# Kernel tuning notes

Measured on AMD Instinct MI355X. Metric: run time of the kernel, lower is better.

Reference implementation:

```python
import jax, jax.numpy as jnp
import numpy as np

EMBED_DIM = 512
N_QUERY = 4096
N_PROTO = 1024


def setup_inputs() -> dict:
    key = jax.random.key(0)
    k_q, k_p, k_wmu = jax.random.split(key, 3)
    d = EMBED_DIM
    bound = (6.0 / (d + d)) ** 0.5
    return {
        "query_features": jax.random.normal(k_q, (N_QUERY, d), dtype=jnp.float32),
        "prototypes": jax.random.normal(k_p, (N_PROTO, d), dtype=jnp.float32),
        "weight_mu": jax.random.uniform(k_wmu, (d, d), dtype=jnp.float32, minval=-bound, maxval=bound),
        "weight_rho": jnp.full((d, d), -3.0, dtype=jnp.float32),
        "bias_mu": jnp.zeros((d,), dtype=jnp.float32),
        "bias_rho": jnp.full((d,), 0.01, dtype=jnp.float32),
        "n_samples": 10,
    }


def reference(query_features, prototypes, weight_mu, weight_rho, bias_mu, bias_rho, n_samples):
    d = weight_mu.shape[0]
    # softplus reparameterization (same each iteration in the original loop)
    weight_sigma = jnp.log1p(jnp.exp(weight_rho))  # [d, d]
    bias_sigma = jnp.log1p(jnp.exp(bias_rho))      # [d]
    # batched MC weight/bias samples: [S, d, d] and [S, d]
    key = jax.random.key(42)
    kw, kb = jax.random.split(key)
    eps_w = jax.random.normal(kw, (n_samples, d, d), dtype=weight_mu.dtype)
    eps_b = jax.random.normal(kb, (n_samples, d), dtype=bias_mu.dtype)
    w = weight_mu[None] + weight_sigma[None] * eps_w   # [S, d, d]
    b = bias_mu[None] + bias_sigma[None] * eps_b       # [S, d]
    # F.linear(x, W_sample.T, b) == x @ W_sample + b
    tq = jnp.einsum('qd,sde->sqe', query_features, w) + b[:, None, :]  # [S, Q, d]
    # cdist via ||a||^2 + ||b||^2 - 2 a.b
    sq_q = jnp.sum(tq * tq, axis=-1)                    # [S, Q]
    sq_p = jnp.sum(prototypes * prototypes, axis=-1)    # [P]
    cross = jnp.einsum('sqe,pe->sqp', tq, prototypes)   # [S, Q, P]
    sqd = sq_q[:, :, None] + sq_p[None, None, :] - 2.0 * cross
    dists = jnp.sqrt(jnp.maximum(sqd, 1e-12))           # [S, Q, P]
    mean_distance = jnp.mean(dists, axis=0)
    uncertainty = jnp.std(dists, axis=0, ddof=1)        # torch.std is unbiased
    return mean_distance, uncertainty
```

## Files before the change

kernel.cpp:

```cpp
#include <hip/hip_runtime.h>
#include <stdint.h>

#define NS 10
#define DIM 512
#define NQ 4096
#define NP 1024

typedef unsigned short ushort_t;
typedef __bf16 bf16el_t;
typedef bf16el_t bf16x8 __attribute__((ext_vector_type(8)));
typedef float floatx4 __attribute__((ext_vector_type(4)));

__host__ __device__ __forceinline__ uint32_t rotl32(uint32_t x, int r) {
  return (x << r) | (x >> (32 - r));
}

__host__ __device__ __forceinline__ void threefry2x32(uint32_t k0, uint32_t k1,
                                                      uint32_t x0, uint32_t x1,
                                                      uint32_t* o0, uint32_t* o1) {
  uint32_t ks2 = k0 ^ k1 ^ 0x1BD11BDAu;
  x0 += k0; x1 += k1;
#define TF_R(r) { x0 += x1; x1 = rotl32(x1, r); x1 ^= x0; }
  TF_R(13) TF_R(15) TF_R(26) TF_R(6)   x0 += k1;  x1 += ks2 + 1u;
  TF_R(17) TF_R(29) TF_R(16) TF_R(24)  x0 += ks2; x1 += k0 + 2u;
  TF_R(13) TF_R(15) TF_R(26) TF_R(6)   x0 += k0;  x1 += k1 + 3u;
  TF_R(17) TF_R(29) TF_R(16) TF_R(24)  x0 += k1;  x1 += ks2 + 4u;
  TF_R(13) TF_R(15) TF_R(26) TF_R(6)   x0 += ks2; x1 += k0 + 5u;
#undef TF_R
  *o0 = x0; *o1 = x1;
}

__device__ __forceinline__ uint32_t jax_random_bits(uint32_t k0, uint32_t k1, uint32_t idx) {
  uint32_t o0, o1;
  threefry2x32(k0, k1, 0u, idx, &o0, &o1);
  return o0 ^ o1;
}

__device__ __forceinline__ float erfinvf_xla(float x) {
  float w = -log1pf(-x * x);
  float p;
  if (w < 5.0f) {
    w -= 2.5f;
    p = 2.81022636e-08f;
    p = fmaf(p, w, 3.43273939e-07f);
    p = fmaf(p, w, -3.5233877e-06f);
    p = fmaf(p, w, -4.39150654e-06f);
    p = fmaf(p, w, 0.00021858087f);
    p = fmaf(p, w, -0.00125372503f);
    p = fmaf(p, w, -0.00417768164f);
    p = fmaf(p, w, 0.246640727f);
    p = fmaf(p, w, 1.50140941f);
  } else {
    w = sqrtf(w) - 3.0f;
    p = -0.000200214257f;
    p = fmaf(p, w, 0.000100950558f);
    p = fmaf(p, w, 0.00134934322f);
    p = fmaf(p, w, -0.00367342844f);
    p = fmaf(p, w, 0.00573950773f);
    p = fmaf(p, w, -0.0076224613f);
    p = fmaf(p, w, 0.00943887047f);
    p = fmaf(p, w, 1.00167406f);
    p = fmaf(p, w, 2.83297682f);
  }
  return p * x;
}

__device__ __forceinline__ float jax_bits_to_normal(uint32_t bits) {
  float f = __uint_as_float((bits >> 9) | 0x3F800000u) - 1.0f;
  float u = f * 2.0f - 0.99999994f;
  u = fmaxf(u, -0.99999994f);
  return 1.41421356f * erfinvf_xla(u);
}

__device__ __forceinline__ float softplusf(float x) { return log1pf(expf(x)); }

__device__ __forceinline__ float bf2f(ushort_t u) {
  return __uint_as_float(((uint32_t)u) << 16);
}
__device__ __forceinline__ ushort_t f2bf(float f) {
  uint32_t u = __float_as_uint(f);
  u += 0x7FFFu + ((u >> 16) & 1u);
  return (ushort_t)(u >> 16);
}

__device__ __forceinline__ void gll16(const void* g, void* l) {
  __builtin_amdgcn_global_load_lds(
      (const __attribute__((address_space(1))) uint32_t*)g,
      (__attribute__((address_space(3))) uint32_t*)l, 16, 0, 0);
}

__global__ __launch_bounds__(256) void prep_kernel(const float* __restrict__ qf,
                                                   const float* __restrict__ pf,
                                                   const float* __restrict__ wmu,
                                                   const float* __restrict__ wrho,
                                                   const float* __restrict__ bmu,
                                                   const float* __restrict__ brho,
                                                   ushort_t* __restrict__ wt,
                                                   ushort_t* __restrict__ qb,
                                                   ushort_t* __restrict__ pb,
                                                   float* __restrict__ sqp,
                                                   float* __restrict__ bvec,
                                                   float* __restrict__ sqq,
                                                   uint32_t kw0, uint32_t kw1,
                                                   uint32_t kb0, uint32_t kb1) {
  const int blk = blockIdx.x;
  const int tid = threadIdx.x;
  if (blk < 10240) {
    uint32_t t = blk * 256u + tid;
    uint32_t s = t >> 18;
    uint32_t r = t & 0x3FFFFu;
    uint32_t e = r >> 9;
    uint32_t k = r & 511u;
    uint32_t eps_idx = (s << 18) | (k << 9) | e;
    uint32_t bits = jax_random_bits(kw0, kw1, eps_idx);
    float n = jax_bits_to_normal(bits);
    uint32_t mi = (k << 9) | e;
    float w = wmu[mi] + softplusf(wrho[mi]) * n;
    wt[t] = f2bf(w);
  } else if (blk < 12288) {
    int i = ((blk - 10240) * 256 + tid) * 4;
    float4 v = *(const float4*)&qf[i];
    uint2 r;
    r.x = (uint32_t)f2bf(v.x) | ((uint32_t)f2bf(v.y) << 16);
    r.y = (uint32_t)f2bf(v.z) | ((uint32_t)f2bf(v.w) << 16);
    *(uint2*)&qb[i] = r;
  } else if (blk < 12544) {
    int p = (blk - 12288) * 4 + (tid >> 6);
    int lane = tid & 63;
    const float* src = pf + p * DIM + lane * 8;
    float4 a = *(const float4*)src;
    float4 b = *(const float4*)(src + 4);
    float vals[8] = {a.x, a.y, a.z, a.w, b.x, b.y, b.z, b.w};
    ushort_t o[8];
    float ss = 0.f;
#pragma unroll
    for (int i = 0; i < 8; ++i) {
      o[i] = f2bf(vals[i]);
      float f = bf2f(o[i]);
      ss += f * f;
    }
    *(uint4*)&pb[p * DIM + lane * 8] = *(const uint4*)o;
#pragma unroll
    for (int off = 32; off; off >>= 1) ss += __shfl_xor(ss, off, 64);
    if (lane == 0) sqp[p] = ss;
  } else if (blk < 12564) {
    uint32_t t2 = (blk - 12544) * 256u + tid;
    uint32_t e = t2 & 511u;
    uint32_t bits = jax_random_bits(kb0, kb1, t2);
    float n = jax_bits_to_normal(bits);
    bvec[t2] = bmu[e] + softplusf(brho[e]) * n;
  } else {
    int i = (blk - 12564) * 256 + tid;
    sqq[i] = 0.f;
  }
}

__global__ __launch_bounds__(256) void gemm_tq_kernel(const ushort_t* __restrict__ qb,
                                                      const ushort_t* __restrict__ wt,
                                                      const float* __restrict__ bvec,
                                                      ushort_t* __restrict__ tq,
                                                      float* __restrict__ sqq) {
  __shared__ __align__(16) ushort_t ls[3 * 128 * 64];
  ushort_t* lsA = ls;
  const int lane = threadIdx.x & 63;
  const int wave = threadIdx.x >> 6;
  const int wm = wave >> 1, wn = wave & 1;
  const int qBase = blockIdx.x * 128;
  const int eBase = blockIdx.y * 128;
  const int s0 = blockIdx.z * 2;
  const int srow = lane >> 3;
  const int scol = ((lane & 7) ^ srow) * 16;
  const char* gA = (const char*)qb + (size_t)(qBase + wave * 32 + srow) * (DIM * 2) + scol;
  const char* gB0 = (const char*)(wt + (size_t)s0 * (DIM * DIM)) +
                    (size_t)(eBase + wave * 32 + srow) * (DIM * 2) + scol;
  const char* gB1 = gB0 + (size_t)(DIM * DIM) * 2;
  char* lA = (char*)&ls[0 * 8192 + wave * 32 * 64];
  char* lB0 = (char*)&ls[1 * 8192 + wave * 32 * 64];
  char* lB1 = (char*)&ls[2 * 8192 + wave * 32 * 64];
  const int cn = lane & 15;
  const int cn7 = cn & 7;
  const int jc = lane >> 4;
  const floatx4 fzero = {0.f, 0.f, 0.f, 0.f};
  floatx4 acc[2][4][4];
#pragma unroll
  for (int sp = 0; sp < 2; ++sp)
#pragma unroll
    for (int mi = 0; mi < 4; ++mi)
#pragma unroll
      for (int ni = 0; ni < 4; ++ni) acc[sp][mi][ni] = fzero;

  for (int kt = 0; kt < 8; ++kt) {
    __syncthreads();
#pragma unroll
    for (int j = 0; j < 4; ++j) {
      gll16(gA + (size_t)j * 8 * (DIM * 2), lA + j * 1024);
      gll16(gB0 + (size_t)j * 8 * (DIM * 2), lB0 + j * 1024);
      gll16(gB1 + (size_t)j * 8 * (DIM * 2), lB1 + j * 1024);
    }
    gA += 128; gB0 += 128; gB1 += 128;
    __syncthreads();
#pragma unroll
    for (int c = 0; c < 8; c += 4) {
      const int po = ((c + jc) ^ cn7) << 3;
      bf16x8 aF[4];
#pragma unroll
      for (int mi = 0; mi < 4; ++mi)
        aF[mi] = *(const bf16x8*)&ls[(wm * 64 + mi * 16 + cn) * 64 + po];
#pragma unroll
      for (int sp = 0; sp < 2; ++sp) {
        bf16x8 bF[4];
#pragma unroll
        for (int ni = 0; ni < 4; ++ni)
          bF[ni] = *(const bf16x8*)&ls[(1 + sp) * 8192 + (wn * 64 + ni * 16 + cn) * 64 + po];
#pragma unroll
        for (int mi = 0; mi < 4; ++mi)
#pragma unroll
          for (int ni = 0; ni < 4; ++ni)
            acc[sp][mi][ni] =
                __builtin_amdgcn_mfma_f32_16x16x32_bf16(aF[mi], bF[ni], acc[sp][mi][ni], 0, 0, 0);
      }
    }
  }

  const int jc4 = jc * 4;
  const int rr = lane >> 3;
  const int ch = lane & 7;
  const int physc = ch ^ rr;
#pragma unroll
  for (int sp = 0; sp < 2; ++sp) {
    const int s = s0 + sp;
    ushort_t* area = ls + wave * 4096;
    float bv[4];
#pragma unroll
    for (int ni = 0; ni < 4; ++ni) bv[ni] = bvec[s * DIM + eBase + wn * 64 + ni * 16 + cn];
    __syncthreads();
#pragma unroll
    for (int mi = 0; mi < 4; ++mi)
#pragma unroll
      for (int ni = 0; ni < 4; ++ni)
#pragma unroll
        for (int r = 0; r < 4; ++r) {
          const int lr = mi * 16 + jc4 + r;
          const int lc = ni * 16 + cn;
          const int off = lr * 64 + (((lc >> 3) ^ (lr & 7)) << 3) + (lc & 7);
          area[off] = f2bf(acc[sp][mi][ni][r] + bv[ni]);
        }
    __syncthreads();
    const size_t tqs = (size_t)s * (NQ * DIM);
#pragma unroll
    for (int pass = 0; pass < 8; ++pass) {
      const int lr = pass * 8 + rr;
      uint4 v = *(const uint4*)&area[lr * 64 + physc * 8];
      uint32_t wsv[4] = {v.x, v.y, v.z, v.w};
      float ss = 0.f;
#pragma unroll
      for (int i = 0; i < 4; ++i) {
        float lo = bf2f((ushort_t)(wsv[i] & 0xFFFFu));
        float hi = bf2f((ushort_t)(wsv[i] >> 16));
        ss += lo * lo + hi * hi;
      }
      ss += __shfl_xor(ss, 1, 64);
      ss += __shfl_xor(ss, 2, 64);
      ss += __shfl_xor(ss, 4, 64);
      const int q = qBase + wm * 64 + lr;
      *(uint4*)&tq[tqs + (size_t)q * DIM + eBase + wn * 64 + ch * 8] = v;
      if (ch == 0) atomicAdd(&sqq[s * NQ + q], ss);
    }
  }
}

__global__ __launch_bounds__(256) void gemm_dist_kernel(const ushort_t* __restrict__ tq,
                                                        const ushort_t* __restrict__ pb,
                                                        const float* __restrict__ sqq,
                                                        const float* __restrict__ sqp,
                                                        float* __restrict__ out) {
  __shared__ __align__(16) ushort_t lsA[64 * 128];
  __shared__ __align__(16) ushort_t lsB[128 * 128];
  const int lane = threadIdx.x & 63;
  const int wave = threadIdx.x >> 6;
  const int wm = wave >> 1;
  const int wn = wave & 1;
  const int qBase = blockIdx.y * 64;
  const int pBase = blockIdx.x * 128;
  const int srow = lane >> 4;
  const int scc = lane & 15;
  const int sccx = scc ^ srow;
  const char* gA = (const char*)tq + (size_t)(qBase + wave * 16 + srow) * (DIM * 2);
  const char* gB = (const char*)pb + (size_t)(pBase + wave * 32 + srow) * (DIM * 2);
  char* lA = (char*)lsA + wave * 4096;
  char* lB = (char*)lsB + wave * 8192;
  const int cn = lane & 15;
  const int jc = lane >> 4;
  const int rq = jc * 4;
  const floatx4 fzero = {0.f, 0.f, 0.f, 0.f};

  float sum[2][4][4] = {};
  float ssq[2][4][4] = {};
  float sqp_v[4];
#pragma unroll
  for (int ni = 0; ni < 4; ++ni) sqp_v[ni] = sqp[pBase + wn * 64 + ni * 16 + cn];

  for (int s = 0; s < NS; ++s) {
    floatx4 acc[2][4];
#pragma unroll
    for (int mi = 0; mi < 2; ++mi)
#pragma unroll
      for (int ni = 0; ni < 4; ++ni) acc[mi][ni] = fzero;

    for (int kt = 0; kt < 4; ++kt) {
      __syncthreads();
#pragma unroll
      for (int g = 0; g < 4; ++g)
        gll16(gA + (size_t)g * 4 * (DIM * 2) + ((sccx ^ (g * 4)) << 4), lA + g * 1024);
#pragma unroll
      for (int g = 0; g < 8; ++g)
        gll16(gB + (size_t)g * 4 * (DIM * 2) + ((sccx ^ ((g & 3) * 4)) << 4), lB + g * 1024);
      gA += 256; gB += 256;
      __syncthreads();
#pragma unroll
      for (int c4 = 0; c4 < 4; ++c4) {
        const int po = (((c4 * 4 + jc) ^ cn) & 15) << 3;
        bf16x8 aF[2], bF[4];
#pragma unroll
        for (int mi = 0; mi < 2; ++mi)
          aF[mi] = *(const bf16x8*)&lsA[(wm * 32 + mi * 16 + cn) * 128 + po];
#pragma unroll
        for (int ni = 0; ni < 4; ++ni)
          bF[ni] = *(const bf16x8*)&lsB[(wn * 64 + ni * 16 + cn) * 128 + po];
#pragma unroll
        for (int mi = 0; mi < 2; ++mi)
#pragma unroll
          for (int ni = 0; ni < 4; ++ni)
            acc[mi][ni] = __builtin_amdgcn_mfma_f32_16x16x32_bf16(aF[mi], bF[ni], acc[mi][ni], 0, 0, 0);
      }
    }
    gA += (size_t)NQ * DIM * 2 - 1024;
    gB -= 1024;
#pragma unroll
    for (int mi = 0; mi < 2; ++mi) {
      float4 aqv = *(const float4*)&sqq[s * NQ + qBase + wm * 32 + mi * 16 + rq];
      float aqa[4] = {aqv.x, aqv.y, aqv.z, aqv.w};
#pragma unroll
      for (int r = 0; r < 4; ++r) {
        float aq = aqa[r];
#pragma unroll
        for (int ni = 0; ni < 4; ++ni) {
          float sqd = fmaxf(fmaf(-2.0f, acc[mi][ni][r], aq + sqp_v[ni]), 1e-12f);
          sum[mi][ni][r] += sqrtf(sqd);
          ssq[mi][ni][r] += sqd;
        }
      }
    }
  }
#pragma unroll
  for (int mi = 0; mi < 2; ++mi)
#pragma unroll
    for (int ni = 0; ni < 4; ++ni)
#pragma unroll
      for (int r = 0; r < 4; ++r) {
        int q = qBase + wm * 32 + mi * 16 + rq + r;
        int p = pBase + wn * 64 + ni * 16 + cn;
        float sm = sum[mi][ni][r];
        float mean = sm * 0.1f;
        float var = (ssq[mi][ni][r] - sm * sm * 0.1f) * (1.0f / 9.0f);
        out[(size_t)q * NP + p] = mean;
        out[(size_t)NQ * NP + (size_t)q * NP + p] = sqrtf(fmaxf(var, 0.0f));
      }
}

extern "C" void kernel_launch(void* const* d_in, const int* in_sizes, int n_in,
                              void* d_out, int out_size, void* d_ws, size_t ws_size,
                              hipStream_t stream) {
  const float* qf   = (const float*)d_in[0];
  const float* pf   = (const float*)d_in[1];
  const float* wmu  = (const float*)d_in[2];
  const float* wrho = (const float*)d_in[3];
  const float* bmu  = (const float*)d_in[4];
  const float* brho = (const float*)d_in[5];
  float* out = (float*)d_out;
  char* ws = (char*)d_ws;
  ushort_t* wt   = (ushort_t*)(ws);
  ushort_t* qb   = (ushort_t*)(ws + 5242880);
  ushort_t* pb   = (ushort_t*)(ws + 9437184);
  float*    bvec = (float*)   (ws + 10485760);
  float*    sqp  = (float*)   (ws + 10506240);
  ushort_t* tq   = (ushort_t*)(ws + 10510336);
  float*    sqq  = (float*)   (ws + 52453376);

  uint32_t kw0, kw1, kb0, kb1;
  threefry2x32(0u, 42u, 0u, 0u, &kw0, &kw1);
  threefry2x32(0u, 42u, 0u, 1u, &kb0, &kb1);

  hipLaunchKernelGGL(prep_kernel, dim3(12724), dim3(256), 0, stream,
                     qf, pf, wmu, wrho, bmu, brho, wt, qb, pb, sqp, bvec, sqq,
                     kw0, kw1, kb0, kb1);
  hipLaunchKernelGGL(gemm_tq_kernel, dim3(32, 4, 5), dim3(256), 0, stream, qb, wt, bvec, tq, sqq);
  hipLaunchKernelGGL(gemm_dist_kernel, dim3(8, 64), dim3(256), 0, stream, tq, pb, sqq, sqp, out);
}
```

Before: 237.7 us.

## Rebalance sample reuse between tq GEMM and distance GEMM, swap grid order

The tq GEMM now computes one MC sample per block, doubling its grid in z and halving its LDS use and accumulator registers. This trades reuse of the query tile for more blocks and higher occupancy. The distance GEMM now processes two samples per k-loop, loading the prototype tile once for both samples and doubling the A tile in LDS. Its grid is also transposed so that consecutive blocks walk along queries, which changes which tiles neighbouring blocks share in L2.

Result: slower. 245.2 us (+3.1%).

```diff
diff --git a/kernel.cpp b/kernel.cpp
--- a/kernel.cpp
+++ b/kernel.cpp
@@ -160,112 +160,99 @@
                                                       const float* __restrict__ bvec,
                                                       ushort_t* __restrict__ tq,
                                                       float* __restrict__ sqq) {
-  __shared__ __align__(16) ushort_t ls[3 * 128 * 64];
+  __shared__ __align__(16) ushort_t ls[2 * 128 * 64];
   ushort_t* lsA = ls;
+  ushort_t* lsB = ls + 128 * 64;
   const int lane = threadIdx.x & 63;
   const int wave = threadIdx.x >> 6;
   const int wm = wave >> 1, wn = wave & 1;
   const int qBase = blockIdx.x * 128;
   const int eBase = blockIdx.y * 128;
-  const int s0 = blockIdx.z * 2;
+  const int s = blockIdx.z;
+  const ushort_t* wbase = wt + (size_t)s * (DIM * DIM);
   const int srow = lane >> 3;
   const int scol = ((lane & 7) ^ srow) * 16;
   const char* gA = (const char*)qb + (size_t)(qBase + wave * 32 + srow) * (DIM * 2) + scol;
-  const char* gB0 = (const char*)(wt + (size_t)s0 * (DIM * DIM)) +
-                    (size_t)(eBase + wave * 32 + srow) * (DIM * 2) + scol;
-  const char* gB1 = gB0 + (size_t)(DIM * DIM) * 2;
-  char* lA = (char*)&ls[0 * 8192 + wave * 32 * 64];
-  char* lB0 = (char*)&ls[1 * 8192 + wave * 32 * 64];
-  char* lB1 = (char*)&ls[2 * 8192 + wave * 32 * 64];
+  const char* gB = (const char*)wbase + (size_t)(eBase + wave * 32 + srow) * (DIM * 2) + scol;
+  char* lA = (char*)&lsA[wave * 32 * 64];
+  char* lB = (char*)&lsB[wave * 32 * 64];
   const int cn = lane & 15;
   const int cn7 = cn & 7;
   const int jc = lane >> 4;
   const floatx4 fzero = {0.f, 0.f, 0.f, 0.f};
-  floatx4 acc[2][4][4];
-#pragma unroll
-  for (int sp = 0; sp < 2; ++sp)
-#pragma unroll
-    for (int mi = 0; mi < 4; ++mi)
-#pragma unroll
-      for (int ni = 0; ni < 4; ++ni) acc[sp][mi][ni] = fzero;
+  floatx4 acc[4][4];
+#pragma unroll
+  for (int mi = 0; mi < 4; ++mi)
+#pragma unroll
+    for (int ni = 0; ni < 4; ++ni) acc[mi][ni] = fzero;
 
   for (int kt = 0; kt < 8; ++kt) {
     __syncthreads();
 #pragma unroll
     for (int j = 0; j < 4; ++j) {
       gll16(gA + (size_t)j * 8 * (DIM * 2), lA + j * 1024);
-      gll16(gB0 + (size_t)j * 8 * (DIM * 2), lB0 + j * 1024);
-      gll16(gB1 + (size_t)j * 8 * (DIM * 2), lB1 + j * 1024);
-    }
-    gA += 128; gB0 += 128; gB1 += 128;
+      gll16(gB + (size_t)j * 8 * (DIM * 2), lB + j * 1024);
+    }
+    gA += 128; gB += 128;
     __syncthreads();
 #pragma unroll
     for (int c = 0; c < 8; c += 4) {
       const int po = ((c + jc) ^ cn7) << 3;
-      bf16x8 aF[4];
+      bf16x8 aF[4], bF[4];
 #pragma unroll
       for (int mi = 0; mi < 4; ++mi)
-        aF[mi] = *(const bf16x8*)&ls[(wm * 64 + mi * 16 + cn) * 64 + po];
-#pragma unroll
-      for (int sp = 0; sp < 2; ++sp) {
-        bf16x8 bF[4];
+        aF[mi] = *(const bf16x8*)&lsA[(wm * 64 + mi * 16 + cn) * 64 + po];
+#pragma unroll
+      for (int ni = 0; ni < 4; ++ni)
+        bF[ni] = *(const bf16x8*)&lsB[(wn * 64 + ni * 16 + cn) * 64 + po];
+#pragma unroll
+      for (int mi = 0; mi < 4; ++mi)
 #pragma unroll
         for (int ni = 0; ni < 4; ++ni)
-          bF[ni] = *(const bf16x8*)&ls[(1 + sp) * 8192 + (wn * 64 + ni * 16 + cn) * 64 + po];
-#pragma unroll
-        for (int mi = 0; mi < 4; ++mi)
-#pragma unroll
-          for (int ni = 0; ni < 4; ++ni)
-            acc[sp][mi][ni] =
-                __builtin_amdgcn_mfma_f32_16x16x32_bf16(aF[mi], bF[ni], acc[sp][mi][ni], 0, 0, 0);
+          acc[mi][ni] = __builtin_amdgcn_mfma_f32_16x16x32_bf16(aF[mi], bF[ni], acc[mi][ni], 0, 0, 0);
+    }
+  }
+
+  __syncthreads();
+  ushort_t* area = ls + wave * 4096;
+  float bv[4];
+#pragma unroll
+  for (int ni = 0; ni < 4; ++ni) bv[ni] = bvec[s * DIM + eBase + wn * 64 + ni * 16 + cn];
+  const int jc4 = jc * 4;
+#pragma unroll
+  for (int mi = 0; mi < 4; ++mi)
+#pragma unroll
+    for (int ni = 0; ni < 4; ++ni)
+#pragma unroll
+      for (int r = 0; r < 4; ++r) {
+        const int lr = mi * 16 + jc4 + r;
+        const int lc = ni * 16 + cn;
+        const int off = lr * 64 + (((lc >> 3) ^ (lr & 7)) << 3) + (lc & 7);
+        area[off] = f2bf(acc[mi][ni][r] + bv[ni]);
       }
-    }
-  }
-
-  const int jc4 = jc * 4;
+  __syncthreads();
   const int rr = lane >> 3;
   const int ch = lane & 7;
   const int physc = ch ^ rr;
-#pragma unroll
-  for (int sp = 0; sp < 2; ++sp) {
-    const int s = s0 + sp;
-    ushort_t* area = ls + wave * 4096;
-    float bv[4];
-#pragma unroll
-    for (int ni = 0; ni < 4; ++ni) bv[ni] = bvec[s * DIM + eBase + wn * 64 + ni * 16 + cn];
-    __syncthreads();
-#pragma unroll
-    for (int mi = 0; mi < 4; ++mi)
-#pragma unroll
-      for (int ni = 0; ni < 4; ++ni)
-#pragma unroll
-        for (int r = 0; r < 4; ++r) {
-          const int lr = mi * 16 + jc4 + r;
-          const int lc = ni * 16 + cn;
-          const int off = lr * 64 + (((lc >> 3) ^ (lr & 7)) << 3) + (lc & 7);
-          area[off] = f2bf(acc[sp][mi][ni][r] + bv[ni]);
-        }
-    __syncthreads();
-    const size_t tqs = (size_t)s * (NQ * DIM);
-#pragma unroll
-    for (int pass = 0; pass < 8; ++pass) {
-      const int lr = pass * 8 + rr;
-      uint4 v = *(const uint4*)&area[lr * 64 + physc * 8];
-      uint32_t wsv[4] = {v.x, v.y, v.z, v.w};
-      float ss = 0.f;
-#pragma unroll
-      for (int i = 0; i < 4; ++i) {
-        float lo = bf2f((ushort_t)(wsv[i] & 0xFFFFu));
-        float hi = bf2f((ushort_t)(wsv[i] >> 16));
-        ss += lo * lo + hi * hi;
-      }
-      ss += __shfl_xor(ss, 1, 64);
-      ss += __shfl_xor(ss, 2, 64);
-      ss += __shfl_xor(ss, 4, 64);
-      const int q = qBase + wm * 64 + lr;
-      *(uint4*)&tq[tqs + (size_t)q * DIM + eBase + wn * 64 + ch * 8] = v;
-      if (ch == 0) atomicAdd(&sqq[s * NQ + q], ss);
-    }
+  const size_t tqs = (size_t)s * (NQ * DIM);
+#pragma unroll
+  for (int pass = 0; pass < 8; ++pass) {
+    const int lr = pass * 8 + rr;
+    uint4 v = *(const uint4*)&area[lr * 64 + physc * 8];
+    uint32_t wsv[4] = {v.x, v.y, v.z, v.w};
+    float ss = 0.f;
+#pragma unroll
+    for (int i = 0; i < 4; ++i) {
+      float lo = bf2f((ushort_t)(wsv[i] & 0xFFFFu));
+      float hi = bf2f((ushort_t)(wsv[i] >> 16));
+      ss += lo * lo + hi * hi;
+    }
+    ss += __shfl_xor(ss, 1, 64);
+    ss += __shfl_xor(ss, 2, 64);
+    ss += __shfl_xor(ss, 4, 64);
+    const int q = qBase + wm * 64 + lr;
+    *(uint4*)&tq[tqs + (size_t)q * DIM + eBase + wn * 64 + ch * 8] = v;
+    if (ch == 0) atomicAdd(&sqq[s * NQ + q], ss);
   }
 }
 
@@ -274,19 +261,19 @@
                                                         const float* __restrict__ sqq,
                                                         const float* __restrict__ sqp,
                                                         float* __restrict__ out) {
-  __shared__ __align__(16) ushort_t lsA[64 * 128];
+  __shared__ __align__(16) ushort_t lsA[2 * 64 * 128];
   __shared__ __align__(16) ushort_t lsB[128 * 128];
   const int lane = threadIdx.x & 63;
   const int wave = threadIdx.x >> 6;
   const int wm = wave >> 1;
   const int wn = wave & 1;
-  const int qBase = blockIdx.y * 64;
-  const int pBase = blockIdx.x * 128;
+  const int qBase = blockIdx.x * 64;
+  const int pBase = blockIdx.y * 128;
   const int srow = lane >> 4;
   const int scc = lane & 15;
   const int sccx = scc ^ srow;
-  const char* gA = (const char*)tq + (size_t)(qBase + wave * 16 + srow) * (DIM * 2);
-  const char* gB = (const char*)pb + (size_t)(pBase + wave * 32 + srow) * (DIM * 2);
+  const char* gAb = (const char*)tq + (size_t)(qBase + wave * 16 + srow) * (DIM * 2);
+  const char* gBb = (const char*)pb + (size_t)(pBase + wave * 32 + srow) * (DIM * 2);
   char* lA = (char*)lsA + wave * 4096;
   char* lB = (char*)lsB + wave * 8192;
   const int cn = lane & 15;
@@ -300,54 +287,70 @@
 #pragma unroll
   for (int ni = 0; ni < 4; ++ni) sqp_v[ni] = sqp[pBase + wn * 64 + ni * 16 + cn];
 
-  for (int s = 0; s < NS; ++s) {
-    floatx4 acc[2][4];
-#pragma unroll
-    for (int mi = 0; mi < 2; ++mi)
-#pragma unroll
-      for (int ni = 0; ni < 4; ++ni) acc[mi][ni] = fzero;
-
+  for (int s0 = 0; s0 < NS; s0 += 2) {
+    floatx4 acc[2][2][4];
+#pragma unroll
+    for (int sp = 0; sp < 2; ++sp)
+#pragma unroll
+      for (int mi = 0; mi < 2; ++mi)
+#pragma unroll
+        for (int ni = 0; ni < 4; ++ni) acc[sp][mi][ni] = fzero;
+
+    const char* gA0 = gAb + (size_t)s0 * (NQ * DIM * 2);
+    const char* gA1 = gA0 + (size_t)(NQ * DIM * 2);
+    const char* gBk = gBb;
     for (int kt = 0; kt < 4; ++kt) {
       __syncthreads();
 #pragma unroll
-      for (int g = 0; g < 4; ++g)
-        gll16(gA + (size_t)g * 4 * (DIM * 2) + ((sccx ^ (g * 4)) << 4), lA + g * 1024);
+      for (int g = 0; g < 4; ++g) {
+        const size_t off = (size_t)g * 4 * (DIM * 2) + (size_t)((sccx ^ (g * 4)) << 4);
+        gll16(gA0 + off, lA + g * 1024);
+        gll16(gA1 + off, lA + 16384 + g * 1024);
+      }
 #pragma unroll
       for (int g = 0; g < 8; ++g)
-        gll16(gB + (size_t)g * 4 * (DIM * 2) + ((sccx ^ ((g & 3) * 4)) << 4), lB + g * 1024);
-      gA += 256; gB += 256;
+        gll16(gBk + (size_t)g * 4 * (DIM * 2) + (size_t)((sccx ^ ((g & 3) * 4)) << 4),
+              lB + g * 1024);
+      gA0 += 256; gA1 += 256; gBk += 256;
       __syncthreads();
 #pragma unroll
       for (int c4 = 0; c4 < 4; ++c4) {
         const int po = (((c4 * 4 + jc) ^ cn) & 15) << 3;
-        bf16x8 aF[2], bF[4];
-#pragma unroll
-        for (int mi = 0; mi < 2; ++mi)
-          aF[mi] = *(const bf16x8*)&lsA[(wm * 32 + mi * 16 + cn) * 128 + po];
+        bf16x8 bF[4];
 #pragma unroll
         for (int ni = 0; ni < 4; ++ni)
           bF[ni] = *(const bf16x8*)&lsB[(wn * 64 + ni * 16 + cn) * 128 + po];
 #pragma unroll
-        for (int mi = 0; mi < 2; ++mi)
-#pragma unroll
-          for (int ni = 0; ni < 4; ++ni)
-            acc[mi][ni] = __builtin_amdgcn_mfma_f32_16x16x32_bf16(aF[mi], bF[ni], acc[mi][ni], 0, 0, 0);
+        for (int sp = 0; sp < 2; ++sp) {
+          bf16x8 aF[2];
+#pragma unroll
+          for (int mi = 0; mi < 2; ++mi)
+            aF[mi] = *(const bf16x8*)&lsA[sp * 8192 + (wm * 32 + mi * 16 + cn) * 128 + po];
+#pragma unroll
+          for (int mi = 0; mi < 2; ++mi)
+#pragma unroll
+            for (int ni = 0; ni < 4; ++ni)
+              acc[sp][mi][ni] =
+                  __builtin_amdgcn_mfma_f32_16x16x32_bf16(aF[mi], bF[ni], acc[sp][mi][ni], 0, 0, 0);
+        }
       }
     }
-    gA += (size_t)NQ * DIM * 2 - 1024;
-    gB -= 1024;
-#pragma unroll
-    for (int mi = 0; mi < 2; ++mi) {
-      float4 aqv = *(const float4*)&sqq[s * NQ + qBase + wm * 32 + mi * 16 + rq];
-      float aqa[4] = {aqv.x, aqv.y, aqv.z, aqv.w};
-#pragma unroll
-      for (int r = 0; r < 4; ++r) {
-        float aq = aqa[r];
-#pragma unroll
-        for (int ni = 0; ni < 4; ++ni) {
-          float sqd = fmaxf(fmaf(-2.0f, acc[mi][ni][r], aq + sqp_v[ni]), 1e-12f);
-          sum[mi][ni][r] += sqrtf(sqd);
-          ssq[mi][ni][r] += sqd;
+#pragma unroll
+    for (int sp = 0; sp < 2; ++sp) {
+      const int s = s0 + sp;
+#pragma unroll
+      for (int mi = 0; mi < 2; ++mi) {
+        float4 aqv = *(const float4*)&sqq[s * NQ + qBase + wm * 32 + mi * 16 + rq];
+        float aqa[4] = {aqv.x, aqv.y, aqv.z, aqv.w};
+#pragma unroll
+        for (int r = 0; r < 4; ++r) {
+          float aq = aqa[r];
+#pragma unroll
+          for (int ni = 0; ni < 4; ++ni) {
+            float sqd = fmaxf(fmaf(-2.0f, acc[sp][mi][ni][r], aq + sqp_v[ni]), 1e-12f);
+            sum[mi][ni][r] += sqrtf(sqd);
+            ssq[mi][ni][r] += sqd;
+          }
         }
       }
     }
@@ -394,6 +397,6 @@
   hipLaunchKernelGGL(prep_kernel, dim3(12724), dim3(256), 0, stream,
                      qf, pf, wmu, wrho, bmu, brho, wt, qb, pb, sqp, bvec, sqq,
                      kw0, kw1, kb0, kb1);
-  hipLaunchKernelGGL(gemm_tq_kernel, dim3(32, 4, 5), dim3(256), 0, stream, qb, wt, bvec, tq, sqq);
-  hipLaunchKernelGGL(gemm_dist_kernel, dim3(8, 64), dim3(256), 0, stream, tq, pb, sqq, sqp, out);
-}
+  hipLaunchKernelGGL(gemm_tq_kernel, dim3(32, 4, 10), dim3(256), 0, stream, qb, wt, bvec, tq, sqq);
+  hipLaunchKernelGGL(gemm_dist_kernel, dim3(64, 8), dim3(256), 0, stream, tq, pb, sqq, sqp, out);
+}
```
